# Kernel tuning notes

Measured on AMD Instinct MI355X. Metric: run time of the kernel, lower is better.

## Reference

```python
import jax, jax.numpy as jnp
import numpy as np

N, C, SUBVEC, K, DOUT, DEPTH = 16384, 64, 16, 16, 1024, 4


def setup_inputs() -> dict:
    key = jax.random.key(0)
    k1, k2, k3, k4, k5 = jax.random.split(key, 5)
    x = jax.random.normal(k1, (N, C * SUBVEC), dtype=jnp.float32)
    split_idxs = jax.random.randint(k2, (C, DEPTH), 0, SUBVEC, dtype=jnp.int32)
    split_vals = jax.random.normal(k3, (C, DEPTH, K // 2), dtype=jnp.float32)
    lookup_tables = jax.random.normal(k4, (C, K, DOUT), dtype=jnp.float32)
    bias = jax.random.normal(k5, (DOUT,), dtype=jnp.float32)
    return {"x": x, "split_idxs": split_idxs, "split_vals": split_vals,
            "lookup_tables": lookup_tables, "bias": bias}


def _encode(x_sub, split_idxs, split_vals):
    # x_sub: (n, C, subvec_len); split_idxs: (C, 4); split_vals: (C, 4, 8)
    n = x_sub.shape[0]
    c_idx = jnp.arange(C)
    enc = jnp.zeros((n, C), dtype=jnp.int32)
    for t in range(DEPTH):  # fixed tree depth 4
        xv = x_sub[:, c_idx, split_idxs[:, t]]            # (n, C) selected feature per codebook
        thresh = split_vals[c_idx[None, :], t, enc]       # (n, C) per-node threshold
        enc = 2 * enc + (xv > thresh).astype(jnp.int32)
    return enc  # values in [0, 16)


def reference(x, split_idxs, split_vals, lookup_tables, bias):
    n = x.shape[0]
    x_sub = x.reshape(n, C, SUBVEC)
    enc = _encode(x_sub, split_idxs, split_vals)           # (n, C) int32
    onehot = jax.nn.one_hot(enc, K, dtype=x.dtype)         # (n, C, K)
    out = jnp.einsum('nck,cko->no', onehot, lookup_tables) # sum over codebooks of LUT rows
    return out + bias
```

## Files before the change

kernel.cpp:

```cpp
#include <hip/hip_runtime.h>

#define NN    16384
#define CBN   64
#define SUBV  16
#define KCODE 16
#define DOUTN 1024
#define DEP   4

typedef short bf16x8 __attribute__((ext_vector_type(8)));
typedef float f32x16 __attribute__((ext_vector_type(16)));

static __device__ __forceinline__ unsigned short f2bf(float f) {
  unsigned int u = __float_as_uint(f);
  u += 0x7FFFu + ((u >> 16) & 1u);
  return (unsigned short)(u >> 16);
}

static __device__ __forceinline__ void gld16(const void* g, void* l) {
  __builtin_amdgcn_global_load_lds(
      (const __attribute__((address_space(1))) unsigned int*)g,
      (__attribute__((address_space(3))) unsigned int*)(uintptr_t)l, 16, 0, 0);
}

__global__ __launch_bounds__(256) void prep_k(
    const float* __restrict__ x, const int* __restrict__ split_idxs,
    const float* __restrict__ split_vals, const float* __restrict__ Tg,
    unsigned char* __restrict__ codes, unsigned int* __restrict__ Tswz) {
  const int t = threadIdx.x;

  if (blockIdx.x < 64) {
    const int img = blockIdx.x;
    const int g = img >> 3, ch = img & 7;
    unsigned int* dst = Tswz + (size_t)img * 8192;
    const int colq = t & 31, kp = (t >> 5) & 7;
    #pragma unroll
    for (int cl = 0; cl < 8; ++cl) {
      const float* g0 = Tg + ((size_t)((ch * 8 + cl) * KCODE + 2 * kp)) * DOUTN
                        + g * 128 + colq * 4;
      float4 r0 = *(const float4*)g0;
      float4 r1 = *(const float4*)(g0 + DOUTN);
      unsigned int pk[4] = {
        f2bf(r0.x) | ((unsigned int)f2bf(r1.x) << 16),
        f2bf(r0.y) | ((unsigned int)f2bf(r1.y) << 16),
        f2bf(r0.z) | ((unsigned int)f2bf(r1.z) << 16),
        f2bf(r0.w) | ((unsigned int)f2bf(r1.w) << 16)};
      unsigned key = (unsigned)(colq & 7) << 2;
      #pragma unroll
      for (int j = 0; j < 4; ++j)
        dst[cl * 1024 + ((((unsigned)(colq * 4 + j)) * 8 + (unsigned)kp) ^ key)]
            = pk[j];
    }
    return;
  }

  __shared__ float xs[8][SUBV * CBN];
  __shared__ int   sidxT[DEP * CBN];
  __shared__ float svalT[DEP * (KCODE / 2) * CBN];
  if (t < DEP * CBN) {
    int d = t >> 6, c = t & 63;
    sidxT[t] = split_idxs[c * DEP + d];
  }
  for (int i = t; i < DEP * (KCODE / 2) * CBN; i += 256) {
    int c = i & 63, de = i >> 6, d = de >> 3, e = de & 7;
    svalT[i] = split_vals[(c * DEP + d) * (KCODE / 2) + e];
  }
  const int n0 = (blockIdx.x - 64) * 8;
  const float4* xg = (const float4*)(x + (size_t)n0 * DOUTN);
  #pragma unroll
  for (int i = 0; i < 8; ++i) {
    int li = t + i * 256;
    int r = li >> 8, cpos = li & 255;
    float4 v = xg[r * 256 + cpos];
    int c = cpos >> 2, s0 = (cpos & 3) * 4, m = (c >> 1) & 15;
    float* row = &xs[r][c * SUBV];
    row[(s0 + 0) ^ m] = v.x; row[(s0 + 1) ^ m] = v.y;
    row[(s0 + 2) ^ m] = v.z; row[(s0 + 3) ^ m] = v.w;
  }
  __syncthreads();
  const int c = t & 63, rg = t >> 6, m = (c >> 1) & 15;
  #pragma unroll
  for (int i = 0; i < 2; ++i) {
    int nl = rg * 2 + i;
    int e = 0;
    #pragma unroll
    for (int d = 0; d < DEP; ++d) {
      float xv = xs[nl][c * SUBV + (sidxT[d * 64 + c] ^ m)];
      float th = svalT[(d * 8 + e) * 64 + c];
      e = 2 * e + (xv > th ? 1 : 0);
    }
    codes[(size_t)(n0 + nl) * CBN + c] = (unsigned char)e;
  }
}

__global__ __launch_bounds__(256, 4) void maddness_mfma(
    const unsigned int* __restrict__ Tswz, const float* __restrict__ bias,
    const unsigned char* __restrict__ codes, float* __restrict__ out) {
  __shared__ __align__(16) unsigned int Tb[2][4096];

  const int t = threadIdx.x;
  const int wid = t >> 6, lane = t & 63, lrow = lane & 31, h = lane >> 5;
  const int g16 = blockIdx.x, g8 = g16 >> 1, half = g16 & 1;
  const int n0 = blockIdx.y * 256;
  const char* img = (const char*)Tswz + (size_t)g8 * 8 * 32768;

  #define STAGE(CH, BUF)                                                     \
    {                                                                        \
      const char* src_ = img + (CH) * 32768;                                 \
      _Pragma("unroll")                                                      \
      for (int i_ = 0; i_ < 4; ++i_) {                                       \
        int seg_ = wid * 4 + i_;                                             \
        gld16(src_ + (seg_ >> 1) * 4096 + half * 2048 + (seg_ & 1) * 1024    \
                  + lane * 16,                                               \
              (char*)&Tb[(BUF)][0] + seg_ * 1024);                           \
      }                                                                      \
    }

  STAGE(0, 0);

  f32x16 acc[2][2];
  #pragma unroll
  for (int rt = 0; rt < 2; ++rt)
    #pragma unroll
    for (int ct = 0; ct < 2; ++ct)
      #pragma unroll
      for (int e = 0; e < 16; ++e) acc[rt][ct][e] = 0.f;

  const unsigned char* crow = codes + (size_t)(n0 + wid * 64 + lrow) * CBN;

  __syncthreads();

  #pragma unroll
  for (int ch = 0; ch < 8; ++ch) {
    const int buf = ch & 1;
    unsigned long long qw[2];
    #pragma unroll
    for (int rt = 0; rt < 2; ++rt)
      qw[rt] = *(const unsigned long long*)(crow + (size_t)rt * 32 * CBN + ch * 8);
    if (ch < 7) STAGE(ch + 1, buf ^ 1);
    const unsigned short* tb = (const unsigned short*)&Tb[buf][0];
    __builtin_amdgcn_s_setprio(1);
    #pragma unroll
    for (int cl = 0; cl < 8; ++cl) {
      bf16x8 bv[2];
      #pragma unroll
      for (int ct = 0; ct < 2; ++ct) {
        unsigned col_loc = (unsigned)(ct * 32 + lrow);
        unsigned uidx = (unsigned)(cl * 1024)
                      + ((col_loc * 16 + (unsigned)h * 8)
                         ^ (((col_loc >> 2) & 7u) << 3));
        bv[ct] = *(const bf16x8*)(tb + uidx);
      }
      #pragma unroll
      for (int rt = 0; rt < 2; ++rt) {
        int c = (int)((qw[rt] >> (8 * cl)) & 255);
        int p = c >> 1;
        unsigned s = 0x3F80u << ((c & 1) << 4);
        union { unsigned int u[4]; bf16x8 v; } A;
        #pragma unroll
        for (int j = 0; j < 4; ++j) A.u[j] = (p == h * 4 + j) ? s : 0u;
        acc[rt][0] = __builtin_amdgcn_mfma_f32_32x32x16_bf16(A.v, bv[0], acc[rt][0], 0, 0, 0);
        acc[rt][1] = __builtin_amdgcn_mfma_f32_32x32x16_bf16(A.v, bv[1], acc[rt][1], 0, 0, 0);
      }
    }
    __builtin_amdgcn_s_setprio(0);
    __syncthreads();
  }

  #pragma unroll
  for (int ct = 0; ct < 2; ++ct) {
    const int col = g16 * 64 + ct * 32 + lrow;
    const float bval = bias[col];
    #pragma unroll
    for (int rt = 0; rt < 2; ++rt)
      #pragma unroll
      for (int r = 0; r < 16; ++r) {
        int row = n0 + wid * 64 + rt * 32 + (r & 3) + 8 * (r >> 2) + 4 * h;
        out[(size_t)row * DOUTN + col] = acc[rt][ct][r] + bval;
      }
  }
}

extern "C" void kernel_launch(void* const* d_in, const int* in_sizes, int n_in,
                              void* d_out, int out_size, void* d_ws, size_t ws_size,
                              hipStream_t stream) {
  const float* x    = (const float*)d_in[0];
  const int*   sidx = (const int*)d_in[1];
  const float* sval = (const float*)d_in[2];
  const float* Tg   = (const float*)d_in[3];
  const float* bias = (const float*)d_in[4];
  float* out = (float*)d_out;
  unsigned char* codes = (unsigned char*)d_ws;
  unsigned int*  Tswz  = (unsigned int*)((char*)d_ws + (1 << 20));

  prep_k<<<64 + NN / 8, 256, 0, stream>>>(x, sidx, sval, Tg, codes, Tswz);
  maddness_mfma<<<dim3(16, 64), 256, 0, stream>>>(Tswz, bias, codes, out);
}
```

Baseline: 53.01 us.

## Load full LUT slice once per 1024-thread block and vectorize prep LDS stores

The MFMA kernel now uses 1024-thread blocks that each cover 1024 rows. Each block loads its entire 128 KB bf16 LUT slice into LDS up front, which removes the per-chunk double-buffered staging and the per-chunk barriers. Codes are prefetched one chunk ahead in registers. The prep kernel writes x into LDS with a float4 swizzle instead of four scalar stores. The trade-off is 128 KB of LDS per block, which allows at most one block per CU, so there is no overlap of load latency with compute at the start.

```diff
diff --git a/kernel.cpp b/kernel.cpp
--- a/kernel.cpp
+++ b/kernel.cpp
@@ -53,7 +53,7 @@
     return;
   }
 
-  __shared__ float xs[8][SUBV * CBN];
+  __shared__ __align__(16) float xs[8][SUBV * CBN];
   __shared__ int   sidxT[DEP * CBN];
   __shared__ float svalT[DEP * (KCODE / 2) * CBN];
   if (t < DEP * CBN) {
@@ -71,20 +71,19 @@
     int li = t + i * 256;
     int r = li >> 8, cpos = li & 255;
     float4 v = xg[r * 256 + cpos];
-    int c = cpos >> 2, s0 = (cpos & 3) * 4, m = (c >> 1) & 15;
-    float* row = &xs[r][c * SUBV];
-    row[(s0 + 0) ^ m] = v.x; row[(s0 + 1) ^ m] = v.y;
-    row[(s0 + 2) ^ m] = v.z; row[(s0 + 3) ^ m] = v.w;
+    int c = cpos >> 2, q = cpos & 3;
+    *(float4*)&xs[r][c * SUBV + ((q ^ (c & 3)) << 2)] = v;
   }
   __syncthreads();
-  const int c = t & 63, rg = t >> 6, m = (c >> 1) & 15;
+  const int c = t & 63, rg = t >> 6;
   #pragma unroll
   for (int i = 0; i < 2; ++i) {
     int nl = rg * 2 + i;
     int e = 0;
     #pragma unroll
     for (int d = 0; d < DEP; ++d) {
-      float xv = xs[nl][c * SUBV + (sidxT[d * 64 + c] ^ m)];
+      int si = sidxT[d * 64 + c];
+      float xv = xs[nl][c * SUBV + (((si >> 2) ^ (c & 3)) << 2) + (si & 3)];
       float th = svalT[(d * 8 + e) * 64 + c];
       e = 2 * e + (xv > th ? 1 : 0);
     }
@@ -92,30 +91,24 @@
   }
 }
 
-__global__ __launch_bounds__(256, 4) void maddness_mfma(
+__global__ __launch_bounds__(1024, 4) void maddness_mfma(
     const unsigned int* __restrict__ Tswz, const float* __restrict__ bias,
     const unsigned char* __restrict__ codes, float* __restrict__ out) {
-  __shared__ __align__(16) unsigned int Tb[2][4096];
+  __shared__ __align__(16) unsigned int Tb[32768];
 
   const int t = threadIdx.x;
   const int wid = t >> 6, lane = t & 63, lrow = lane & 31, h = lane >> 5;
   const int g16 = blockIdx.x, g8 = g16 >> 1, half = g16 & 1;
-  const int n0 = blockIdx.y * 256;
+  const int n0 = blockIdx.y * 1024;
   const char* img = (const char*)Tswz + (size_t)g8 * 8 * 32768;
 
-  #define STAGE(CH, BUF)                                                     \
-    {                                                                        \
-      const char* src_ = img + (CH) * 32768;                                 \
-      _Pragma("unroll")                                                      \
-      for (int i_ = 0; i_ < 4; ++i_) {                                       \
-        int seg_ = wid * 4 + i_;                                             \
-        gld16(src_ + (seg_ >> 1) * 4096 + half * 2048 + (seg_ & 1) * 1024    \
-                  + lane * 16,                                               \
-              (char*)&Tb[(BUF)][0] + seg_ * 1024);                           \
-      }                                                                      \
-    }
-
-  STAGE(0, 0);
+  #pragma unroll
+  for (int i = 0; i < 8; ++i) {
+    int gs = wid * 8 + i;
+    int ch = gs >> 4, s16 = gs & 15, cl = s16 >> 1, pc = s16 & 1;
+    gld16(img + ch * 32768 + cl * 4096 + half * 2048 + pc * 1024 + lane * 16,
+          (char*)Tb + gs * 1024);
+  }
 
   f32x16 acc[2][2];
   #pragma unroll
@@ -126,18 +119,19 @@
       for (int e = 0; e < 16; ++e) acc[rt][ct][e] = 0.f;
 
   const unsigned char* crow = codes + (size_t)(n0 + wid * 64 + lrow) * CBN;
+  unsigned long long qwA[2], qwB[2];
+  qwA[0] = *(const unsigned long long*)(crow);
+  qwA[1] = *(const unsigned long long*)(crow + 32 * CBN);
 
   __syncthreads();
 
   #pragma unroll
   for (int ch = 0; ch < 8; ++ch) {
-    const int buf = ch & 1;
-    unsigned long long qw[2];
-    #pragma unroll
-    for (int rt = 0; rt < 2; ++rt)
-      qw[rt] = *(const unsigned long long*)(crow + (size_t)rt * 32 * CBN + ch * 8);
-    if (ch < 7) STAGE(ch + 1, buf ^ 1);
-    const unsigned short* tb = (const unsigned short*)&Tb[buf][0];
+    if (ch < 7) {
+      qwB[0] = *(const unsigned long long*)(crow + (ch + 1) * 8);
+      qwB[1] = *(const unsigned long long*)(crow + 32 * CBN + (ch + 1) * 8);
+    }
+    const unsigned short* tb = (const unsigned short*)Tb + ch * 8192;
     __builtin_amdgcn_s_setprio(1);
     #pragma unroll
     for (int cl = 0; cl < 8; ++cl) {
@@ -152,7 +146,7 @@
       }
       #pragma unroll
       for (int rt = 0; rt < 2; ++rt) {
-        int c = (int)((qw[rt] >> (8 * cl)) & 255);
+        int c = (int)((qwA[rt] >> (8 * cl)) & 255);
         int p = c >> 1;
         unsigned s = 0x3F80u << ((c & 1) << 4);
         union { unsigned int u[4]; bf16x8 v; } A;
@@ -163,7 +157,7 @@
       }
     }
     __builtin_amdgcn_s_setprio(0);
-    __syncthreads();
+    qwA[0] = qwB[0]; qwA[1] = qwB[1];
   }
 
   #pragma unroll
@@ -193,5 +187,5 @@
   unsigned int*  Tswz  = (unsigned int*)((char*)d_ws + (1 << 20));
 
   prep_k<<<64 + NN / 8, 256, 0, stream>>>(x, sidx, sval, Tg, codes, Tswz);
-  maddness_mfma<<<dim3(16, 64), 256, 0, stream>>>(Tswz, bias, codes, out);
+  maddness_mfma<<<dim3(16, 16), 1024, 0, stream>>>(Tswz, bias, codes, out);
 }
```

Measured after the change: 52.82 us. About the same (-0.4%).
